# Performance work log

Measured on AMD Instinct MI355X. Metric: run time of the kernel, lower is better.

Reference implementation:

```python
import jax, jax.numpy as jnp
import numpy as np

N, NFEAT, NHID, NCLASS, NHEAD = 8192, 512, 64, 16, 4
ALPHA = 0.1  # leaky relu slope
NEG = -9e15


def setup_inputs() -> dict:
    key = jax.random.key(0)
    ks = jax.random.split(key, 7)
    x = jax.random.normal(ks[0], (N, NFEAT), dtype=jnp.float32)
    adj = (jax.random.uniform(ks[1], (N, N)) < 0.05).astype(jnp.float32)
    # per-head params: W [H, nfeat, nhid], a [H, 2*nhid] (xavier-ish scale)
    W = jax.random.normal(ks[2], (NHEAD, NFEAT, NHID), dtype=jnp.float32) * (1.0 / np.sqrt(NFEAT))
    a = jax.random.normal(ks[3], (NHEAD, 2 * NHID), dtype=jnp.float32) * (1.0 / np.sqrt(NHID))
    W_out = jax.random.normal(ks[4], (NHEAD * NHID, NCLASS), dtype=jnp.float32) * (1.0 / np.sqrt(NHEAD * NHID))
    a_out = jax.random.normal(ks[5], (2 * NCLASS,), dtype=jnp.float32) * (1.0 / np.sqrt(NCLASS))
    return {"x": x, "adj": adj, "W": W, "a": a, "W_out": W_out, "a_out": a_out}


def _gat_layer(h, adj, Wk, ak):
    """Dense pyGAT GraphAttentionLayer (eval mode, dropout = identity)."""
    d = Wk.shape[1]
    Wh = h @ Wk                         # [N, d]
    f1 = Wh @ ak[:d]                    # [N]
    f2 = Wh @ ak[d:]                    # [N]
    e = jax.nn.leaky_relu(f1[:, None] + f2[None, :], negative_slope=ALPHA)  # [N, N]
    att = jax.nn.softmax(jnp.where(adj > 0, e, NEG), axis=1)
    return att @ Wh                     # [N, d]


def reference(x, adj, W, a, W_out, a_out):
    # eval mode: F.dropout is identity
    heads = jax.vmap(lambda Wk, ak: jax.nn.elu(_gat_layer(x, adj, Wk, ak)))(W, a)  # [H, N, nhid]
    h = jnp.transpose(heads, (1, 0, 2)).reshape(x.shape[0], -1)                    # [N, H*nhid]
    out = jax.nn.elu(_gat_layer(h, adj, W_out, a_out))                             # [N, nclass]
    return jax.nn.log_softmax(out, axis=1)
```

## Files before the change

kernel.cpp:

```cpp
#include <hip/hip_runtime.h>
#include <hip/hip_bf16.h>

#define NN 8192
#define NFEAT 512
#define NHID 64
#define NCLASS 16
#define NHEAD 4
#define ALPHA 0.1f
#define CAP 768

typedef short bf16x4 __attribute__((ext_vector_type(4)));
typedef short bf16x8 __attribute__((ext_vector_type(8)));

__device__ __forceinline__ float lrelu(float x) { return fmaxf(x, ALPHA * x); }
__device__ __forceinline__ float elu(float x) { return x > 0.f ? x : __expf(x) - 1.f; }
__device__ __forceinline__ short f2b(float x) {
  union { __bf16 b; short s; } c; c.b = (__bf16)x; return c.s;
}
__device__ __forceinline__ float b2f(short x) {
  union { unsigned int u; float f; } c; c.u = ((unsigned int)(unsigned short)x) << 16; return c.f;
}

__global__ __launch_bounds__(256) void k_gemm1(const float* __restrict__ x,
                                               const float* __restrict__ W,
                                               float* __restrict__ Wh) {
  __shared__ float As[16][65];
  __shared__ float Bs[16][65];
  const int bm = blockIdx.x * 64;
  const int h  = blockIdx.y;
  const int tid = threadIdx.x;
  const int tx = tid & 15, ty = tid >> 4;
  float acc[4][4] = {};
  for (int k0 = 0; k0 < NFEAT; k0 += 16) {
    {
      int m = tid >> 2;
      int kk = (tid & 3) * 4;
      const float4 xa = *reinterpret_cast<const float4*>(&x[(size_t)(bm + m) * NFEAT + k0 + kk]);
      As[kk + 0][m] = xa.x; As[kk + 1][m] = xa.y; As[kk + 2][m] = xa.z; As[kk + 3][m] = xa.w;
      int c = tid & 63;
      int kb = (tid >> 6) * 4;
#pragma unroll
      for (int u = 0; u < 4; ++u)
        Bs[kb + u][c] = W[((size_t)h * NFEAT + (k0 + kb + u)) * NHID + c];
    }
    __syncthreads();
#pragma unroll
    for (int kk2 = 0; kk2 < 16; ++kk2) {
      float av[4], bv[4];
#pragma unroll
      for (int u = 0; u < 4; ++u) { av[u] = As[kk2][ty * 4 + u]; bv[u] = Bs[kk2][tx * 4 + u]; }
#pragma unroll
      for (int i2 = 0; i2 < 4; ++i2)
#pragma unroll
        for (int j2 = 0; j2 < 4; ++j2) acc[i2][j2] += av[i2] * bv[j2];
    }
    __syncthreads();
  }
#pragma unroll
  for (int i2 = 0; i2 < 4; ++i2)
#pragma unroll
    for (int j2 = 0; j2 < 4; ++j2)
      Wh[((size_t)h * NN + bm + ty * 4 + i2) * NHID + tx * 4 + j2] = acc[i2][j2];
}

__global__ __launch_bounds__(256) void k_f12(const float* __restrict__ Wh,
                                             const float* __restrict__ a,
                                             float* __restrict__ f1,
                                             float* __restrict__ f2,
                                             short* __restrict__ WhB) {
  int wid = blockIdx.x * 4 + (threadIdx.x >> 6);
  int lane = threadIdx.x & 63;
  int h = wid >> 13;
  int i = wid & (NN - 1);
  float v = Wh[((size_t)h * NN + i) * NHID + lane];
  WhB[(size_t)i * (NHEAD * NHID) + h * NHID + lane] = f2b(v);
  float s1 = v * a[h * 2 * NHID + lane];
  float s2 = v * a[h * 2 * NHID + NHID + lane];
#pragma unroll
  for (int off = 32; off; off >>= 1) { s1 += __shfl_xor(s1, off); s2 += __shfl_xor(s2, off); }
  if (lane == 0) { f1[h * NN + i] = s1; f2[h * NN + i] = s2; }
}

__global__ __launch_bounds__(256) void k_rmax(const float* __restrict__ src,
                                              float* __restrict__ dst, int n) {
  const float* p = src + (size_t)blockIdx.x * n;
  float m = -1e30f;
  for (int k = threadIdx.x; k < n; k += 256) m = fmaxf(m, p[k]);
#pragma unroll
  for (int off = 32; off; off >>= 1) m = fmaxf(m, __shfl_xor(m, off));
  __shared__ float sm[4];
  if ((threadIdx.x & 63) == 0) sm[threadIdx.x >> 6] = m;
  __syncthreads();
  if (threadIdx.x == 0) dst[blockIdx.x] = fmaxf(fmaxf(sm[0], sm[1]), fmaxf(sm[2], sm[3]));
}

__global__ __launch_bounds__(256) void k_attn1(const float* __restrict__ adj,
                                               const short* __restrict__ WhB,
                                               const float* __restrict__ f1,
                                               const float* __restrict__ f2,
                                               const float* __restrict__ f2max,
                                               short* __restrict__ hcat,
                                               unsigned int* __restrict__ bmask) {
  __shared__ unsigned short idx[CAP];
  __shared__ float wl[NHEAD][CAP];
  __shared__ float red[4][NHEAD * NHID];
  __shared__ float swp[4][NHEAD];
  __shared__ float sinv[NHEAD];
  __shared__ int cnt;
  const int i = blockIdx.x;
  const int tid = threadIdx.x;
  const int wv = tid >> 6, lane = tid & 63;
  if (tid == 0) cnt = 0;
  __syncthreads();

  const float4* arow = reinterpret_cast<const float4*>(adj + (size_t)i * NN);
  unsigned int* brow = bmask + (size_t)i * (NN / 32);
#pragma unroll
  for (int s = 0; s < 8; ++s) {
    const float4 v = arow[s * 256 + tid];
    const int b0 = v.x > 0.f, b1 = v.y > 0.f, b2 = v.z > 0.f, b3 = v.w > 0.f;
    unsigned int nv = (unsigned int)(b0 | (b1 << 1) | (b2 << 2) | (b3 << 3)) << ((tid & 7) * 4);
    nv |= __shfl_xor(nv, 1); nv |= __shfl_xor(nv, 2); nv |= __shfl_xor(nv, 4);
    if ((tid & 7) == 0) brow[s * 32 + (tid >> 3)] = nv;
    const int c = b0 + b1 + b2 + b3;
    if (c) {
      int base = atomicAdd(&cnt, c);
      const int j = s * 1024 + tid * 4;
      if (b0 && base < CAP) idx[base++] = (unsigned short)j;
      if (b1 && base < CAP) idx[base++] = (unsigned short)(j + 1);
      if (b2 && base < CAP) idx[base++] = (unsigned short)(j + 2);
      if (b3 && base < CAP) idx[base++] = (unsigned short)(j + 3);
    }
  }
  __syncthreads();
  const int n = min(cnt, CAP);

  float f1r[NHEAD], mrow[NHEAD], sw[NHEAD] = {0.f, 0.f, 0.f, 0.f};
#pragma unroll
  for (int h = 0; h < NHEAD; ++h) {
    f1r[h] = f1[h * NN + i];
    mrow[h] = lrelu(f1r[h] + f2max[h]);
  }
  for (int k = tid; k < n; k += 256) {
    const int j = idx[k];
#pragma unroll
    for (int h = 0; h < NHEAD; ++h) {
      const float w = __expf(lrelu(f1r[h] + f2[h * NN + j]) - mrow[h]);
      wl[h][k] = w;
      sw[h] += w;
    }
  }
#pragma unroll
  for (int off = 32; off; off >>= 1)
#pragma unroll
    for (int h = 0; h < NHEAD; ++h) sw[h] += __shfl_xor(sw[h], off);
  if (lane == 0) {
#pragma unroll
    for (int h = 0; h < NHEAD; ++h) swp[wv][h] = sw[h];
  }
  __syncthreads();
  if (tid < NHEAD) sinv[tid] = 1.f / (swp[0][tid] + swp[1][tid] + swp[2][tid] + swp[3][tid]);

  const int g = tid >> 4, gl = tid & 15;
  const int h0 = gl >> 3;
  float accA[8] = {}, accB[8] = {};
#pragma unroll 2
  for (int k = g; k < n; k += 16) {
    const int j = idx[k];
    const float wA = wl[h0][k];
    const float wB = wl[h0 + 2][k];
    const bf16x8 vA = *reinterpret_cast<const bf16x8*>(WhB + (size_t)j * 256 + gl * 8);
    const bf16x8 vB = *reinterpret_cast<const bf16x8*>(WhB + (size_t)j * 256 + 128 + gl * 8);
#pragma unroll
    for (int u = 0; u < 8; ++u) {
      accA[u] += wA * b2f(vA[u]);
      accB[u] += wB * b2f(vB[u]);
    }
  }
#pragma unroll
  for (int u = 0; u < 8; ++u) {
    accA[u] += __shfl_xor(accA[u], 16); accA[u] += __shfl_xor(accA[u], 32);
    accB[u] += __shfl_xor(accB[u], 16); accB[u] += __shfl_xor(accB[u], 32);
  }
  if (lane < 16) {
#pragma unroll
    for (int u = 0; u < 8; ++u) {
      red[wv][gl * 8 + u] = accA[u];
      red[wv][128 + gl * 8 + u] = accB[u];
    }
  }
  __syncthreads();
  {
    const int hc = tid, h = hc >> 6;
    const float s = red[0][hc] + red[1][hc] + red[2][hc] + red[3][hc];
    hcat[(size_t)i * (NHEAD * NHID) + hc] = f2b(elu(s * sinv[h]));
  }
}

__global__ __launch_bounds__(256) void k_gemm2(const short* __restrict__ hcat,
                                               const float* __restrict__ Wout,
                                               const float* __restrict__ aout,
                                               short* __restrict__ Wh2B,
                                               float* __restrict__ f1o,
                                               float* __restrict__ f2o) {
  __shared__ float sW[NHEAD * NHID][NCLASS + 1];
  __shared__ float sh[16][NHEAD * NHID + 1];
  const int tid = threadIdx.x;
  const int r = tid >> 4, c = tid & 15;
  const int row = blockIdx.x * 16 + r;
  for (int u = tid; u < 256 * 16; u += 256) sW[u >> 4][u & 15] = Wout[u];
  for (int u = tid; u < 16 * 256; u += 256)
    sh[u >> 8][u & 255] = b2f(hcat[(size_t)(blockIdx.x * 16 + (u >> 8)) * 256 + (u & 255)]);
  __syncthreads();
  float acc = 0.f;
#pragma unroll 8
  for (int f = 0; f < 256; ++f) acc += sh[r][f] * sW[f][c];
  Wh2B[(size_t)row * NCLASS + c] = f2b(acc);
  float s1 = acc * aout[c];
  float s2 = acc * aout[NCLASS + c];
#pragma unroll
  for (int off = 8; off; off >>= 1) { s1 += __shfl_xor(s1, off); s2 += __shfl_xor(s2, off); }
  if (c == 0) { f1o[row] = s1; f2o[row] = s2; }
}

__global__ __launch_bounds__(256) void k_attn2(const unsigned int* __restrict__ bmask,
                                               const short* __restrict__ Wh2B,
                                               const float* __restrict__ f1o,
                                               const float* __restrict__ f2o,
                                               const float* __restrict__ f2omax,
                                               float* __restrict__ out) {
  __shared__ unsigned short idx[CAP];
  __shared__ float wl[CAP];
  __shared__ float red[4][NCLASS];
  __shared__ float swp[4];
  __shared__ float sinvs;
  __shared__ int cnt;
  const int i = blockIdx.x;
  const int tid = threadIdx.x;
  const int wv = tid >> 6, lane = tid & 63;
  if (tid == 0) cnt = 0;
  __syncthreads();

  {
    unsigned int word = bmask[(size_t)i * (NN / 32) + tid];
    const int c = __popc(word);
    if (c) {
      int base = atomicAdd(&cnt, c);
      const int j0 = tid * 32;
      while (word) {
        const int b = __ffs(word) - 1;
        word &= word - 1;
        if (base < CAP) idx[base++] = (unsigned short)(j0 + b);
      }
    }
  }
  __syncthreads();
  const int n = min(cnt, CAP);

  const float f1r = f1o[i];
  const float mrow = lrelu(f1r + f2omax[0]);
  float sw = 0.f;
  for (int k = tid; k < n; k += 256) {
    const int j = idx[k];
    const float w = __expf(lrelu(f1r + f2o[j]) - mrow);
    wl[k] = w;
    sw += w;
  }
#pragma unroll
  for (int off = 32; off; off >>= 1) sw += __shfl_xor(sw, off);
  if (lane == 0) swp[wv] = sw;
  __syncthreads();
  if (tid == 0) sinvs = 1.f / (swp[0] + swp[1] + swp[2] + swp[3]);

  const int g = tid >> 2, gl = tid & 3;
  float acc[4] = {};
#pragma unroll 2
  for (int k = g; k < n; k += 64) {
    const int j = idx[k];
    const float w = wl[k];
    const bf16x4 v = *reinterpret_cast<const bf16x4*>(Wh2B + (size_t)j * NCLASS + gl * 4);
#pragma unroll
    for (int u = 0; u < 4; ++u) acc[u] += w * b2f(v[u]);
  }
#pragma unroll
  for (int u = 0; u < 4; ++u) {
    acc[u] += __shfl_xor(acc[u], 4);
    acc[u] += __shfl_xor(acc[u], 8);
    acc[u] += __shfl_xor(acc[u], 16);
    acc[u] += __shfl_xor(acc[u], 32);
  }
  if (lane < 4) {
#pragma unroll
    for (int u = 0; u < 4; ++u) red[wv][lane * 4 + u] = acc[u];
  }
  __syncthreads();
  if (tid < NCLASS) {
    const float s = red[0][tid] + red[1][tid] + red[2][tid] + red[3][tid];
    const float v = elu(s * sinvs);
    float vm = v;
#pragma unroll
    for (int off = 8; off; off >>= 1) vm = fmaxf(vm, __shfl_xor(vm, off, 16));
    float ex = __expf(v - vm);
#pragma unroll
    for (int off = 8; off; off >>= 1) ex += __shfl_xor(ex, off, 16);
    out[(size_t)i * NCLASS + tid] = v - vm - __logf(ex);
  }
}

extern "C" void kernel_launch(void* const* d_in, const int* in_sizes, int n_in,
                              void* d_out, int out_size, void* d_ws, size_t ws_size,
                              hipStream_t stream) {
  const float* x    = (const float*)d_in[0];
  const float* adj  = (const float*)d_in[1];
  const float* W    = (const float*)d_in[2];
  const float* a    = (const float*)d_in[3];
  const float* Wout = (const float*)d_in[4];
  const float* aout = (const float*)d_in[5];
  float* out = (float*)d_out;
  char* ws = (char*)d_ws;
  const size_t MB = 1048576;

  float* Wh            = (float*)(ws);
  short* WhB           = (short*)(ws + 8 * MB);
  unsigned int* bmask  = (unsigned int*)(ws + 12 * MB);
  short* hcat          = (short*)(ws + 20 * MB);
  float* f1            = (float*)(ws + 24 * MB);
  float* f2            = (float*)(ws + 24 * MB + 131072);
  float* f1o           = (float*)(ws + 24 * MB + 262144);
  float* f2o           = (float*)(ws + 24 * MB + 294912);
  short* Wh2B          = (short*)(ws + 24 * MB + 327680);
  float* f2max         = (float*)(ws + 24 * MB + 589824);
  float* f2omax        = (float*)(ws + 24 * MB + 589888);

  k_gemm1<<<dim3(NN / 64, NHEAD), 256, 0, stream>>>(x, W, Wh);
  k_f12<<<NN * NHEAD / 4, 256, 0, stream>>>(Wh, a, f1, f2, WhB);
  k_rmax<<<NHEAD, 256, 0, stream>>>(f2, f2max, NN);
  k_attn1<<<NN, 256, 0, stream>>>(adj, WhB, f1, f2, f2max, hcat, bmask);
  k_gemm2<<<NN / 16, 256, 0, stream>>>(hcat, Wout, aout, Wh2B, f1o, f2o);
  k_rmax<<<1, 256, 0, stream>>>(f2o, f2omax, NN);
  k_attn2<<<NN, 256, 0, stream>>>(bmask, Wh2B, f1o, f2o, f2omax, out);
}
```

Baseline: 262.0 us.

## Interleave f2 by node and restructure attention gather to read full rows per group

Stores f2 interleaved as [node][head] so the softmax-weight pass loads all four heads for a neighbor in one float4 instead of four scattered loads, and k_rmax gains stride/offset parameters to match. The head-1 aggregation loop is reworked so that each 8-lane group reads a full 512-byte WhB row (all four heads) per neighbor, with 32 accumulators per lane and the next neighbor index prefetched. bf16 unpacking is done with shift/mask on 32-bit words. k_attn2 gets the same prefetch and unpack treatment. The larger accumulator set raises register pressure, which may reduce occupancy.

New measurement: 282.1 us. +7.6%, slower.

```diff
diff --git a/kernel.cpp b/kernel.cpp
--- a/kernel.cpp
+++ b/kernel.cpp
@@ -9,7 +9,6 @@
 #define ALPHA 0.1f
 #define CAP 768
 
-typedef short bf16x4 __attribute__((ext_vector_type(4)));
 typedef short bf16x8 __attribute__((ext_vector_type(8)));
 
 __device__ __forceinline__ float lrelu(float x) { return fmaxf(x, ALPHA * x); }
@@ -20,6 +19,14 @@
 __device__ __forceinline__ float b2f(short x) {
   union { unsigned int u; float f; } c; c.u = ((unsigned int)(unsigned short)x) << 16; return c.f;
 }
+
+#define UPF(w, v, A0, A1)                                  \
+  {                                                        \
+    const float lo_ = __uint_as_float((v) << 16);          \
+    const float hi_ = __uint_as_float((v) & 0xffff0000u);  \
+    (A0) += (w) * lo_;                                     \
+    (A1) += (w) * hi_;                                     \
+  }
 
 __global__ __launch_bounds__(256) void k_gemm1(const float* __restrict__ x,
                                                const float* __restrict__ W,
@@ -66,7 +73,7 @@
 __global__ __launch_bounds__(256) void k_f12(const float* __restrict__ Wh,
                                              const float* __restrict__ a,
                                              float* __restrict__ f1,
-                                             float* __restrict__ f2,
+                                             float* __restrict__ f2i,
                                              short* __restrict__ WhB) {
   int wid = blockIdx.x * 4 + (threadIdx.x >> 6);
   int lane = threadIdx.x & 63;
@@ -78,14 +85,15 @@
   float s2 = v * a[h * 2 * NHID + NHID + lane];
 #pragma unroll
   for (int off = 32; off; off >>= 1) { s1 += __shfl_xor(s1, off); s2 += __shfl_xor(s2, off); }
-  if (lane == 0) { f1[h * NN + i] = s1; f2[h * NN + i] = s2; }
+  if (lane == 0) { f1[h * NN + i] = s1; f2i[(size_t)i * 4 + h] = s2; }
 }
 
 __global__ __launch_bounds__(256) void k_rmax(const float* __restrict__ src,
-                                              float* __restrict__ dst, int n) {
-  const float* p = src + (size_t)blockIdx.x * n;
+                                              float* __restrict__ dst, int n, int stride,
+                                              int boff) {
+  const float* p = src + (size_t)blockIdx.x * boff;
   float m = -1e30f;
-  for (int k = threadIdx.x; k < n; k += 256) m = fmaxf(m, p[k]);
+  for (int k = threadIdx.x; k < n; k += 256) m = fmaxf(m, p[(size_t)k * stride]);
 #pragma unroll
   for (int off = 32; off; off >>= 1) m = fmaxf(m, __shfl_xor(m, off));
   __shared__ float sm[4];
@@ -97,7 +105,7 @@
 __global__ __launch_bounds__(256) void k_attn1(const float* __restrict__ adj,
                                                const short* __restrict__ WhB,
                                                const float* __restrict__ f1,
-                                               const float* __restrict__ f2,
+                                               const float* __restrict__ f2i,
                                                const float* __restrict__ f2max,
                                                short* __restrict__ hcat,
                                                unsigned int* __restrict__ bmask) {
@@ -143,12 +151,13 @@
   }
   for (int k = tid; k < n; k += 256) {
     const int j = idx[k];
-#pragma unroll
-    for (int h = 0; h < NHEAD; ++h) {
-      const float w = __expf(lrelu(f1r[h] + f2[h * NN + j]) - mrow[h]);
-      wl[h][k] = w;
-      sw[h] += w;
-    }
+    const float4 f = *reinterpret_cast<const float4*>(f2i + (size_t)j * 4);
+    const float w0 = __expf(lrelu(f1r[0] + f.x) - mrow[0]);
+    const float w1 = __expf(lrelu(f1r[1] + f.y) - mrow[1]);
+    const float w2 = __expf(lrelu(f1r[2] + f.z) - mrow[2]);
+    const float w3 = __expf(lrelu(f1r[3] + f.w) - mrow[3]);
+    wl[0][k] = w0; wl[1][k] = w1; wl[2][k] = w2; wl[3][k] = w3;
+    sw[0] += w0; sw[1] += w1; sw[2] += w2; sw[3] += w3;
   }
 #pragma unroll
   for (int off = 32; off; off >>= 1)
@@ -161,39 +170,49 @@
   __syncthreads();
   if (tid < NHEAD) sinv[tid] = 1.f / (swp[0][tid] + swp[1][tid] + swp[2][tid] + swp[3][tid]);
 
-  const int g = tid >> 4, gl = tid & 15;
-  const int h0 = gl >> 3;
-  float accA[8] = {}, accB[8] = {};
-#pragma unroll 2
-  for (int k = g; k < n; k += 16) {
-    const int j = idx[k];
-    const float wA = wl[h0][k];
-    const float wB = wl[h0 + 2][k];
-    const bf16x8 vA = *reinterpret_cast<const bf16x8*>(WhB + (size_t)j * 256 + gl * 8);
-    const bf16x8 vB = *reinterpret_cast<const bf16x8*>(WhB + (size_t)j * 256 + 128 + gl * 8);
-#pragma unroll
-    for (int u = 0; u < 8; ++u) {
-      accA[u] += wA * b2f(vA[u]);
-      accB[u] += wB * b2f(vB[u]);
-    }
-  }
-#pragma unroll
-  for (int u = 0; u < 8; ++u) {
-    accA[u] += __shfl_xor(accA[u], 16); accA[u] += __shfl_xor(accA[u], 32);
-    accB[u] += __shfl_xor(accB[u], 16); accB[u] += __shfl_xor(accB[u], 32);
-  }
-  if (lane < 16) {
-#pragma unroll
-    for (int u = 0; u < 8; ++u) {
-      red[wv][gl * 8 + u] = accA[u];
-      red[wv][128 + gl * 8 + u] = accB[u];
-    }
+  const int g = tid >> 3, l = tid & 7;
+  float acc[32];
+#pragma unroll
+  for (int u = 0; u < 32; ++u) acc[u] = 0.f;
+  int k = g;
+  int jc = (k < n) ? (int)idx[k] : -1;
+  while (jc >= 0) {
+    const int kn = k + 32;
+    const int jn = (kn < n) ? (int)idx[kn] : -1;
+    const uint4* bp = reinterpret_cast<const uint4*>(WhB + (size_t)jc * 256);
+    const uint4 e0 = bp[l];
+    const uint4 e1 = bp[8 + l];
+    const uint4 e2 = bp[16 + l];
+    const uint4 e3 = bp[24 + l];
+    const float w0 = wl[0][k], w1 = wl[1][k], w2 = wl[2][k], w3 = wl[3][k];
+    UPF(w0, e0.x, acc[0], acc[1])   UPF(w0, e0.y, acc[2], acc[3])
+    UPF(w0, e0.z, acc[4], acc[5])   UPF(w0, e0.w, acc[6], acc[7])
+    UPF(w1, e1.x, acc[8], acc[9])   UPF(w1, e1.y, acc[10], acc[11])
+    UPF(w1, e1.z, acc[12], acc[13]) UPF(w1, e1.w, acc[14], acc[15])
+    UPF(w2, e2.x, acc[16], acc[17]) UPF(w2, e2.y, acc[18], acc[19])
+    UPF(w2, e2.z, acc[20], acc[21]) UPF(w2, e2.w, acc[22], acc[23])
+    UPF(w3, e3.x, acc[24], acc[25]) UPF(w3, e3.y, acc[26], acc[27])
+    UPF(w3, e3.z, acc[28], acc[29]) UPF(w3, e3.w, acc[30], acc[31])
+    k = kn; jc = jn;
+  }
+#pragma unroll
+  for (int u = 0; u < 32; ++u) {
+    acc[u] += __shfl_xor(acc[u], 8);
+    acc[u] += __shfl_xor(acc[u], 16);
+    acc[u] += __shfl_xor(acc[u], 32);
+  }
+  if (lane < 8) {
+#pragma unroll
+    for (int q = 0; q < 4; ++q)
+#pragma unroll
+      for (int u = 0; u < 8; ++u)
+        red[wv][q * 64 + l * 8 + u] = acc[q * 8 + u];
   }
   __syncthreads();
   {
-    const int hc = tid, h = hc >> 6;
+    const int hc = tid;
     const float s = red[0][hc] + red[1][hc] + red[2][hc] + red[3][hc];
-    hcat[(size_t)i * (NHEAD * NHID) + hc] = f2b(elu(s * sinv[h]));
+    hcat[(size_t)i * (NHEAD * NHID) + hc] = f2b(elu(s * sinv[hc >> 6]));
   }
 }
 
@@ -274,13 +293,16 @@
 
   const int g = tid >> 2, gl = tid & 3;
   float acc[4] = {};
-#pragma unroll 2
-  for (int k = g; k < n; k += 64) {
-    const int j = idx[k];
+  int k = g;
+  int jc = (k < n) ? (int)idx[k] : -1;
+  while (jc >= 0) {
+    const int kn = k + 64;
+    const int jn = (kn < n) ? (int)idx[kn] : -1;
     const float w = wl[k];
-    const bf16x4 v = *reinterpret_cast<const bf16x4*>(Wh2B + (size_t)j * NCLASS + gl * 4);
-#pragma unroll
-    for (int u = 0; u < 4; ++u) acc[u] += w * b2f(v[u]);
+    const uint2 v = *reinterpret_cast<const uint2*>(Wh2B + (size_t)jc * NCLASS + gl * 4);
+    UPF(w, v.x, acc[0], acc[1])
+    UPF(w, v.y, acc[2], acc[3])
+    k = kn; jc = jn;
   }
 #pragma unroll
   for (int u = 0; u < 4; ++u) {
@@ -325,7 +347,7 @@
   unsigned int* bmask  = (unsigned int*)(ws + 12 * MB);
   short* hcat          = (short*)(ws + 20 * MB);
   float* f1            = (float*)(ws + 24 * MB);
-  float* f2            = (float*)(ws + 24 * MB + 131072);
+  float* f2i           = (float*)(ws + 24 * MB + 131072);
   float* f1o           = (float*)(ws + 24 * MB + 262144);
   float* f2o           = (float*)(ws + 24 * MB + 294912);
   short* Wh2B          = (short*)(ws + 24 * MB + 327680);
@@ -333,10 +355,10 @@
   float* f2omax        = (float*)(ws + 24 * MB + 589888);
 
   k_gemm1<<<dim3(NN / 64, NHEAD), 256, 0, stream>>>(x, W, Wh);
-  k_f12<<<NN * NHEAD / 4, 256, 0, stream>>>(Wh, a, f1, f2, WhB);
-  k_rmax<<<NHEAD, 256, 0, stream>>>(f2, f2max, NN);
-  k_attn1<<<NN, 256, 0, stream>>>(adj, WhB, f1, f2, f2max, hcat, bmask);
+  k_f12<<<NN * NHEAD / 4, 256, 0, stream>>>(Wh, a, f1, f2i, WhB);
+  k_rmax<<<NHEAD, 256, 0, stream>>>(f2i, f2max, NN, 4, 1);
+  k_attn1<<<NN, 256, 0, stream>>>(adj, WhB, f1, f2i, f2max, hcat, bmask);
   k_gemm2<<<NN / 16, 256, 0, stream>>>(hcat, Wout, aout, Wh2B, f1o, f2o);
-  k_rmax<<<1, 256, 0, stream>>>(f2o, f2omax, NN);
+  k_rmax<<<1, 256, 0, stream>>>(f2o, f2omax, NN, 1, 0);
   k_attn2<<<NN, 256, 0, stream>>>(bmask, Wh2B, f1o, f2o, f2omax, out);
 }
```
